# Performance work log

Hardware: AMD Instinct MI355X
Metric: run time of the kernel (lower is better)

The kernel has to match this reference:

```python
import jax, jax.numpy as jnp
import numpy as np

N = 50000        # num nodes
E = 800000       # num edges (no self loops by construction)
D = 128          # in_features == out_features
NE = 4           # num_envs
EPS = 1e-8
STDV = 1.0 / np.sqrt(D)


def setup_inputs() -> dict:
    key = jax.random.key(0)
    k = jax.random.split(key, 6)
    x = jax.random.normal(k[0], (N, D), jnp.float32)
    row = jax.random.randint(k[1], (E,), 0, N, dtype=jnp.int32)
    off = jax.random.randint(k[2], (E,), 1, N, dtype=jnp.int32)
    col = (row + off) % N  # guarantees no self loops (matches remove_self_loops)
    adj = jnp.stack([row, col])
    env_weights = jax.random.uniform(k[3], (N, NE), jnp.float32)
    weights = jax.random.uniform(k[4], (NE, D, D), jnp.float32, -STDV, STDV)
    a = jax.random.normal(k[5], (NE, 2 * D, 1), jnp.float32) * np.sqrt(2.0 / (2 * D + 1)) * 1.414
    return {"x": x, "adj": adj, "env_weights": env_weights, "weights": weights, "a": a}


def reference(x, adj, env_weights, weights, a):
    n = x.shape[0]
    f = weights.shape[-1]
    loops = jnp.arange(n, dtype=adj.dtype)
    src = jnp.concatenate([adj[0], loops])  # add_self_loops
    dst = jnp.concatenate([adj[1], loops])
    # per-env projected features: [NE, N, F]
    h = jnp.einsum('nd,edf->enf', x, weights)
    # attention logits: cat(h[src], h[dst]) @ a  ==  h[src]@a1 + h[dst]@a2
    a1 = a[:, :f, 0]   # [NE, F]
    a2 = a[:, f:, 0]   # [NE, F]
    s_src = jnp.einsum('enf,ef->en', h, a1)
    s_dst = jnp.einsum('enf,ef->en', h, a2)
    logits = jax.nn.leaky_relu(s_src[:, src] + s_dst[:, dst], 0.01)  # [NE, Etot]
    # global per-env max subtraction (as in the torch code: max over all edges)
    e = jnp.exp(logits - jnp.max(logits, axis=1, keepdims=True))
    def agg(ek, hk):
        # specialspmm: out[src] += ek * hk[dst]; denom via ones vector
        denom = jax.ops.segment_sum(ek, src, num_segments=n) + EPS          # [N]
        num = jax.ops.segment_sum(ek[:, None] * hk[dst], src, num_segments=n)  # [N, F]
        return num / denom[:, None]
    out_env = jax.vmap(agg)(e, h)  # [NE, N, F]
    out = jnp.einsum('ne,enf->nf', env_weights, out_env)
    return out + x  # residual
```

## Files before the change

### kernel.cpp

```cpp
#include <hip/hip_runtime.h>

#define N_NODES 50000
#define N_EDGES 800000
#define D_FEAT  128
#define NE_ENV  4
#define EPS_F   1e-8f
#define M_CONST 4.0f
#define NB_BUCKET 391
#define BINA_BLOCKS 250
#define BINA_EPT 13
#define NBH 200
#define EH  4000

typedef __attribute__((ext_vector_type(8))) short bf16x8;
typedef __attribute__((ext_vector_type(4))) float floatx4;
typedef __attribute__((ext_vector_type(2))) float f32x2;

static __device__ __forceinline__ unsigned short f2bf(float v) {
    union { float f; unsigned int u; } c; c.f = v;
    unsigned int u = c.u;
    u += 0x7fffu + ((u >> 16) & 1u);
    return (unsigned short)(u >> 16);
}

static __device__ __forceinline__ f32x2 bf2f(unsigned int v) {
    f32x2 r;
    r.x = __uint_as_float(v << 16);
    r.y = __uint_as_float(v & 0xffff0000u);
    return r;
}

static __device__ __forceinline__ float lrelu_exp(float z) {
    float lk = z > 0.f ? z : 0.01f * z;
    return __expf(lk - M_CONST);
}

static __device__ __forceinline__ void pk_add(f32x2& acc, f32x2 w) {
    asm("v_pk_add_f32 %0, %1, %0" : "+v"(acc) : "v"(w));
}
static __device__ __forceinline__ void pk_fma_bl(f32x2& acc, f32x2 w, f32x2 x) {
    asm("v_pk_fma_f32 %0, %1, %2, %0 op_sel:[0,0,0] op_sel_hi:[0,1,1]" : "+v"(acc) : "v"(w), "v"(x));
}
static __device__ __forceinline__ void pk_fma_bh(f32x2& acc, f32x2 w, f32x2 x) {
    asm("v_pk_fma_f32 %0, %1, %2, %0 op_sel:[1,0,0] op_sel_hi:[1,1,1]" : "+v"(acc) : "v"(w), "v"(x));
}

static __device__ __forceinline__ void edge_acc(unsigned int xv, float4 w,
        f32x2& den01, f32x2& den23, f32x2* axy) {
    f32x2 x = bf2f(xv);
    f32x2 wxy; wxy.x = w.x; wxy.y = w.y;
    f32x2 wzw; wzw.x = w.z; wzw.y = w.w;
    pk_add(den01, wxy);
    pk_add(den23, wzw);
    pk_fma_bl(axy[0], wxy, x);
    pk_fma_bh(axy[1], wxy, x);
    pk_fma_bl(axy[2], wzw, x);
    pk_fma_bh(axy[3], wzw, x);
}

__global__ __launch_bounds__(256) void k_setup(const float* __restrict__ weights, const float* __restrict__ a,
        float* __restrict__ b, unsigned short* __restrict__ wsw,
        const int* __restrict__ row, int* __restrict__ bcnt) {
    int blk = blockIdx.x;
    if (blk < 128) {
        int wave = threadIdx.x >> 6, lane = threadIdx.x & 63;
        int t = blk * 4 + wave;
        int e = t >> 7, d = t & 127;
        float2 w2 = ((const float2*)(weights + e * 16384 + d * 128))[lane];
        float2 a1 = ((const float2*)(a + e * 256))[lane];
        float2 a2 = ((const float2*)(a + e * 256 + 128))[lane];
        float p1 = w2.x * a1.x + w2.y * a1.y;
        float p2 = w2.x * a2.x + w2.y * a2.y;
#pragma unroll
        for (int off = 32; off > 0; off >>= 1) {
            p1 += __shfl_xor(p1, off, 64);
            p2 += __shfl_xor(p2, off, 64);
        }
        if (lane == 0) {
            b[e * 128 + d] = p1;
            b[512 + e * 128 + d] = p2;
        }
    } else if (blk < 384) {
        int idx = (blk - 128) * 256 + threadIdx.x;
        int j = idx & 7;
        int l = (idx >> 3) & 63;
        int t = (idx >> 9) & 7;
        int s = idx >> 12;
        int k = s * 32 + (l >> 4) * 8 + j;
        int f = t * 16 + (l & 15);
        int e = k >> 7, d = k & 127;
        wsw[idx] = f2bf(weights[e * 16384 + d * 128 + f]);
    } else {
        __shared__ int h[NB_BUCKET];
        int t = threadIdx.x;
        for (int i = t; i < NB_BUCKET; i += 256) h[i] = 0;
        __syncthreads();
        int e0 = (blk - 384) * EH;
        for (int j = t; j < EH; j += 256) {
            int k = e0 + j;
            if (k < N_EDGES) atomicAdd(&h[row[k] >> 7], 1);
        }
        __syncthreads();
        for (int i = t; i < NB_BUCKET; i += 256) {
            int c = h[i];
            if (c) atomicAdd(&bcnt[i], c);
        }
    }
}

__global__ __launch_bounds__(256) void k_s(const float* __restrict__ x, const float* __restrict__ b,
        float* __restrict__ s_src, float* __restrict__ s_dst, unsigned short* __restrict__ xbf) {
    int wave = threadIdx.x >> 6, lane = threadIdx.x & 63;
    int gw = blockIdx.x * 4 + wave;
    if (gw >= 3125) return;
    int quad = lane >> 4, lm = lane & 15;
    int base = gw * 16;

    floatx4 acc = (floatx4){0.f, 0.f, 0.f, 0.f};
    const float* xrow = x + (size_t)(base + lm) * 128 + quad * 8;
    unsigned short* xbrow = xbf + (size_t)(base + lm) * 128 + quad * 8;

#pragma unroll
    for (int s = 0; s < 4; ++s) {
        float4 lo = *(const float4*)(xrow + s * 32);
        float4 hi = *(const float4*)(xrow + s * 32 + 4);
        bf16x8 af;
        af[0] = (short)f2bf(lo.x); af[1] = (short)f2bf(lo.y);
        af[2] = (short)f2bf(lo.z); af[3] = (short)f2bf(lo.w);
        af[4] = (short)f2bf(hi.x); af[5] = (short)f2bf(hi.y);
        af[6] = (short)f2bf(hi.z); af[7] = (short)f2bf(hi.w);
        *(bf16x8*)(xbrow + s * 32) = af;

        bf16x8 bfv = (bf16x8){0, 0, 0, 0, 0, 0, 0, 0};
        if (lm < 8) {
            const float* bp = b + lm * 128 + s * 32 + quad * 8;
            float4 b0 = *(const float4*)bp;
            float4 b1 = *(const float4*)(bp + 4);
            bfv[0] = (short)f2bf(b0.x); bfv[1] = (short)f2bf(b0.y);
            bfv[2] = (short)f2bf(b0.z); bfv[3] = (short)f2bf(b0.w);
            bfv[4] = (short)f2bf(b1.x); bfv[5] = (short)f2bf(b1.y);
            bfv[6] = (short)f2bf(b1.z); bfv[7] = (short)f2bf(b1.w);
        }
        acc = __builtin_amdgcn_mfma_f32_16x16x32_bf16(af, bfv, acc, 0, 0, 0);
    }
    if (lm < 8) {
        float* dstp = (lm < 4) ? (s_src + (size_t)(base + quad * 4) * 4 + lm)
                               : (s_dst + (size_t)(base + quad * 4) * 4 + (lm - 4));
#pragma unroll
        for (int r = 0; r < 4; ++r) dstp[r * 4] = acc[r];
    }
}

__global__ void k_bscan(const int* __restrict__ bcnt, int* __restrict__ bbase,
                        int* __restrict__ bcur, int* __restrict__ offsets) {
    __shared__ int sm[512];
    int t = threadIdx.x;
    int v = (t < NB_BUCKET) ? bcnt[t] : 0;
    sm[t] = v;
    __syncthreads();
    for (int s2 = 1; s2 < 512; s2 <<= 1) {
        int add = (t >= s2) ? sm[t - s2] : 0;
        __syncthreads();
        sm[t] += add;
        __syncthreads();
    }
    int excl = sm[t] - v;
    if (t < NB_BUCKET) { bbase[t] = excl; bcur[t] = excl; }
    if (t == NB_BUCKET) bbase[t] = excl;
    if (t == 0) offsets[N_NODES] = N_EDGES;
}

__global__ __launch_bounds__(256) void k_binA(const int* __restrict__ row, const int* __restrict__ col,
        int* __restrict__ bcur, unsigned int* __restrict__ binned) {
    __shared__ int cnt[NB_BUCKET];
    __shared__ int base[NB_BUCKET];
    int t = threadIdx.x;
    for (int b = t; b < NB_BUCKET; b += 256) cnt[b] = 0;
    __syncthreads();
    unsigned int pk[BINA_EPT];
    int ebase = blockIdx.x * (256 * BINA_EPT) + t;
#pragma unroll
    for (int j = 0; j < BINA_EPT; ++j) {
        int k = ebase + j * 256;
        pk[j] = 0xffffffffu;
        if (k < N_EDGES) {
            unsigned int s = (unsigned int)row[k];
            unsigned int d = (unsigned int)col[k];
            pk[j] = (s << 16) | d;
            atomicAdd(&cnt[s >> 7], 1);
        }
    }
    __syncthreads();
    for (int b = t; b < NB_BUCKET; b += 256) {
        int c = cnt[b];
        base[b] = c ? atomicAdd(&bcur[b], c) : 0;
        cnt[b] = 0;
    }
    __syncthreads();
#pragma unroll
    for (int j = 0; j < BINA_EPT; ++j) {
        if (pk[j] != 0xffffffffu) {
            int b = pk[j] >> 23;
            int off = atomicAdd(&cnt[b], 1);
            binned[base[b] + off] = pk[j];
        }
    }
}

__global__ __launch_bounds__(256) void k_binB(const unsigned int* __restrict__ binned,
        const int* __restrict__ bbase,
        const float* __restrict__ s_src, const float* __restrict__ s_dst,
        int* __restrict__ offsets, int* __restrict__ sorted_dst, float4* __restrict__ w_sorted) {
    __shared__ int hist[128];
    __shared__ int cur[128];
    int b = blockIdx.x;
    int nb = b << 7;
    int nc = min(128, N_NODES - nb);
    int t = threadIdx.x;
    if (t < 128) hist[t] = 0;
    __syncthreads();
    int ebeg = bbase[b];
    int eend = bbase[b + 1];
    for (int i = ebeg + t; i < eend; i += 256)
        atomicAdd(&hist[(binned[i] >> 16) & 127], 1);
    __syncthreads();
    int v = (t < 128) ? hist[t] : 0;
    for (int s2 = 1; s2 < 128; s2 <<= 1) {
        int add = (t >= s2 && t < 128) ? hist[t - s2] : 0;
        __syncthreads();
        if (t < 128) hist[t] += add;
        __syncthreads();
    }
    if (t < 128) {
        int pos = ebeg + hist[t] - v;
        cur[t] = pos;
        if (t < nc) offsets[nb + t] = pos;
    }
    __syncthreads();
    for (int i = ebeg + t; i < eend; i += 256) {
        unsigned int pk = binned[i];
        int s = (int)(pk >> 16), d = (int)(pk & 0xffffu);
        float4 a4 = *(const float4*)(s_src + s * 4);
        float4 b4 = *(const float4*)(s_dst + d * 4);
        float4 w;
        w.x = lrelu_exp(a4.x + b4.x);
        w.y = lrelu_exp(a4.y + b4.y);
        w.z = lrelu_exp(a4.z + b4.z);
        w.w = lrelu_exp(a4.w + b4.w);
        int pos = atomicAdd(&cur[s & 127], 1);
        sorted_dst[pos] = d;
        w_sorted[pos] = w;
    }
}

__global__ __launch_bounds__(256) void k_agg_gemm(const unsigned int* __restrict__ xb,
        const float* __restrict__ s_src, const float* __restrict__ s_dst,
        const int* __restrict__ offsets, const int* __restrict__ sorted_dst,
        const float4* __restrict__ w_sorted, const float* __restrict__ env_w,
        const unsigned short* __restrict__ Wsw,
        const float* __restrict__ x, float* __restrict__ out) {
    __shared__ __align__(16) unsigned int Gsm[16 * 256];
    int wave = threadIdx.x >> 6, lane = threadIdx.x & 63;
    int nb = blockIdx.x * 16;

#pragma unroll 1
    for (int j = 0; j < 4; ++j) {
        int r = wave * 4 + j;
        int n = nb + r;

        f32x2 den01, den23;
        f32x2 axy[4];
        {
            float4 sa = *(const float4*)(s_src + n * 4);
            float4 sb = *(const float4*)(s_dst + n * 4);
            float ws0 = lrelu_exp(sa.x + sb.x), ws1 = lrelu_exp(sa.y + sb.y);
            float ws2 = lrelu_exp(sa.z + sb.z), ws3 = lrelu_exp(sa.w + sb.w);
            f32x2 xv = bf2f(xb[((unsigned)n << 6) + lane]);
            den01.x = ws0; den01.y = ws1;
            den23.x = ws2; den23.y = ws3;
            axy[0].x = ws0 * xv.x; axy[0].y = ws0 * xv.y;
            axy[1].x = ws1 * xv.x; axy[1].y = ws1 * xv.y;
            axy[2].x = ws2 * xv.x; axy[2].y = ws2 * xv.y;
            axy[3].x = ws3 * xv.x; axy[3].y = ws3 * xv.y;
        }

        int beg = __builtin_amdgcn_readfirstlane(offsets[n]);
        int end = __builtin_amdgcn_readfirstlane(offsets[n + 1]);
        int i = beg;

        if (i + 15 < end) {
            float4 wA[8]; unsigned int vA[8];
            {
                int dA[8];
#pragma unroll
                for (int q = 0; q < 8; ++q) dA[q] = sorted_dst[i + q];
#pragma unroll
                for (int q = 0; q < 8; ++q) vA[q] = xb[((unsigned)dA[q] << 6) + lane];
#pragma unroll
                for (int q = 0; q < 8; ++q) wA[q] = w_sorted[i + q];
            }
            i += 8;
            for (; i + 7 < end; i += 8) {
                int dB[8]; float4 wB[8]; unsigned int vB[8];
#pragma unroll
                for (int q = 0; q < 8; ++q) dB[q] = sorted_dst[i + q];
#pragma unroll
                for (int q = 0; q < 8; ++q) vB[q] = xb[((unsigned)dB[q] << 6) + lane];
#pragma unroll
                for (int q = 0; q < 8; ++q) wB[q] = w_sorted[i + q];
#pragma unroll
                for (int q = 0; q < 8; ++q) edge_acc(vA[q], wA[q], den01, den23, axy);
#pragma unroll
                for (int q = 0; q < 8; ++q) { vA[q] = vB[q]; wA[q] = wB[q]; }
            }
#pragma unroll
            for (int q = 0; q < 8; ++q) edge_acc(vA[q], wA[q], den01, den23, axy);
        }
        for (; i + 7 < end; i += 8) {
            int d[8]; float4 w[8]; unsigned int v[8];
#pragma unroll
            for (int q = 0; q < 8; ++q) d[q] = sorted_dst[i + q];
#pragma unroll
            for (int q = 0; q < 8; ++q) v[q] = xb[((unsigned)d[q] << 6) + lane];
#pragma unroll
            for (int q = 0; q < 8; ++q) w[q] = w_sorted[i + q];
#pragma unroll
            for (int q = 0; q < 8; ++q) edge_acc(v[q], w[q], den01, den23, axy);
        }
        for (; i + 3 < end; i += 4) {
            int d[4]; float4 w[4]; unsigned int v[4];
#pragma unroll
            for (int q = 0; q < 4; ++q) d[q] = sorted_dst[i + q];
#pragma unroll
            for (int q = 0; q < 4; ++q) v[q] = xb[((unsigned)d[q] << 6) + lane];
#pragma unroll
            for (int q = 0; q < 4; ++q) w[q] = w_sorted[i + q];
#pragma unroll
            for (int q = 0; q < 4; ++q) edge_acc(v[q], w[q], den01, den23, axy);
        }
        for (; i < end; ++i) {
            int d0 = sorted_dst[i];
            edge_acc(xb[((unsigned)d0 << 6) + lane], w_sorted[i], den01, den23, axy);
        }

        float4 ewt = *(const float4*)(env_w + n * 4);
        float ewv[4] = { ewt.x, ewt.y, ewt.z, ewt.w };
        float dens[4] = { den01.x, den01.y, den23.x, den23.y };
        int swz = (r & 7) << 2;
#pragma unroll
        for (int e = 0; e < 4; ++e) {
            float sc = ewv[e] / (dens[e] + EPS_F);
            unsigned int lo = f2bf(sc * axy[e].x);
            unsigned int hi = f2bf(sc * axy[e].y);
            Gsm[(r * 256 + e * 64 + lane) ^ swz] = (hi << 16) | lo;
        }
    }
    __syncthreads();

    int quad = lane >> 4, lm = lane & 15;
    int t0 = wave * 2;
    floatx4 acc0 = (floatx4){0.f, 0.f, 0.f, 0.f};
    floatx4 acc1 = (floatx4){0.f, 0.f, 0.f, 0.f};
    int rswz = (lm & 7) << 2;
#pragma unroll
    for (int s = 0; s < 16; ++s) {
        int idx = (lm * 256 + s * 16 + quad * 4) ^ rswz;
        bf16x8 af = *(const bf16x8*)(&Gsm[idx]);
        bf16x8 b0 = *(const bf16x8*)(Wsw + (((s * 8 + t0) * 64 + lane) * 8));
        bf16x8 b1 = *(const bf16x8*)(Wsw + (((s * 8 + t0 + 1) * 64 + lane) * 8));
        acc0 = __builtin_amdgcn_mfma_f32_16x16x32_bf16(af, b0, acc0, 0, 0, 0);
        acc1 = __builtin_amdgcn_mfma_f32_16x16x32_bf16(af, b1, acc1, 0, 0, 0);
    }
    int row_base = nb + quad * 4;
#pragma unroll
    for (int r = 0; r < 4; ++r) {
        int rowi = row_base + r;
        int c0 = t0 * 16 + lm;
        int c1 = c0 + 16;
        out[rowi * 128 + c0] = acc0[r] + x[rowi * 128 + c0];
        out[rowi * 128 + c1] = acc1[r] + x[rowi * 128 + c1];
    }
}

extern "C" void kernel_launch(void* const* d_in, const int* in_sizes, int n_in,
                              void* d_out, int out_size, void* d_ws, size_t ws_size,
                              hipStream_t stream) {
    const float* x       = (const float*)d_in[0];
    const int*   adj     = (const int*)d_in[1];
    const int*   row     = adj;
    const int*   col     = adj + N_EDGES;
    const float* env_w   = (const float*)d_in[2];
    const float* weights = (const float*)d_in[3];
    const float* a       = (const float*)d_in[4];
    float* out = (float*)d_out;

    char* ws = (char*)d_ws;
    size_t off = 0;
    auto alloc = [&](size_t bytes) -> char* {
        char* p = ws + off;
        off += (bytes + 255) & ~(size_t)255;
        return p;
    };
    float* b          = (float*)alloc(1024 * 4);
    float* s_src      = (float*)alloc((size_t)N_NODES * 4 * 4);
    float* s_dst      = (float*)alloc((size_t)N_NODES * 4 * 4);
    int*   offsets    = (int*)alloc((size_t)(N_NODES + 1) * 4);
    int*   bcnt       = (int*)alloc(512 * 4);
    int*   bbase      = (int*)alloc(512 * 4);
    int*   bcur       = (int*)alloc(512 * 4);
    unsigned int* binned = (unsigned int*)alloc((size_t)N_EDGES * 4);
    int*   sorted_dst = (int*)alloc((size_t)N_EDGES * 4);
    float4* w_sorted  = (float4*)alloc((size_t)N_EDGES * 16);
    unsigned short* wsw = (unsigned short*)alloc(65536 * 2);
    unsigned short* xbf = (unsigned short*)alloc((size_t)N_NODES * 128 * 2);

    hipMemsetAsync(bcnt, 0, 512 * 4, stream);
    k_setup<<<384 + NBH, 256, 0, stream>>>(weights, a, b, wsw, row, bcnt);
    k_s<<<782, 256, 0, stream>>>(x, b, s_src, s_dst, xbf);
    k_bscan<<<1, 512, 0, stream>>>(bcnt, bbase, bcur, offsets);
    k_binA<<<BINA_BLOCKS, 256, 0, stream>>>(row, col, bcur, binned);
    k_binB<<<NB_BUCKET, 256, 0, stream>>>(binned, bbase, s_src, s_dst, offsets, sorted_dst, w_sorted);
    k_agg_gemm<<<3125, 256, 0, stream>>>((const unsigned int*)xbf, s_src, s_dst, offsets,
                                         sorted_dst, w_sorted, env_w, wsw, x, out);
}
```

Before: 185.8 us.

## Fuse bucket scan into setup, double agg-gemm rows per block, scalarize weight pointer

Removes the separate single-block scan kernel by having the last histogram block (detected via an atomic done counter) do the bucket prefix scan. Doubles k_agg_gemm's tile to 32 nodes per block, so each loaded W fragment feeds twice as many MFMAs, and adds bounds guards for the partial last block. Forces the edge-weight base pointer through a VGPR move so the vector loads use a uniform address. Trade-offs: one fewer launch and less W reload traffic, against half as many blocks, fewer waves in flight for latency hiding during the gather, and double the LDS per block.

New measurement: 227.0 us. 22.2% more time.

```diff
diff --git a/kernel.cpp b/kernel.cpp
--- a/kernel.cpp
+++ b/kernel.cpp
@@ -58,9 +58,16 @@
     pk_fma_bh(axy[3], wzw, x);
 }
 
+static __device__ __forceinline__ const float4* wvec_ptr(const float4* w_sorted, int i) {
+    int iv;
+    asm("v_mov_b32 %0, %1" : "=v"(iv) : "s"(i));
+    return (const float4*)((const char*)w_sorted + ((size_t)(unsigned)iv * 16));
+}
+
 __global__ __launch_bounds__(256) void k_setup(const float* __restrict__ weights, const float* __restrict__ a,
         float* __restrict__ b, unsigned short* __restrict__ wsw,
-        const int* __restrict__ row, int* __restrict__ bcnt) {
+        const int* __restrict__ row, int* __restrict__ bcnt, int* __restrict__ done,
+        int* __restrict__ bbase, int* __restrict__ bcur, int* __restrict__ offsets) {
     int blk = blockIdx.x;
     if (blk < 128) {
         int wave = threadIdx.x >> 6, lane = threadIdx.x & 63;
@@ -92,8 +99,9 @@
         wsw[idx] = f2bf(weights[e * 16384 + d * 128 + f]);
     } else {
         __shared__ int h[NB_BUCKET];
+        __shared__ int lastflag;
         int t = threadIdx.x;
-        for (int i = t; i < NB_BUCKET; i += 256) h[i] = 0;
+        for (int i2 = t; i2 < NB_BUCKET; i2 += 256) h[i2] = 0;
         __syncthreads();
         int e0 = (blk - 384) * EH;
         for (int j = t; j < EH; j += 256) {
@@ -101,9 +109,34 @@
             if (k < N_EDGES) atomicAdd(&h[row[k] >> 7], 1);
         }
         __syncthreads();
-        for (int i = t; i < NB_BUCKET; i += 256) {
-            int c = h[i];
-            if (c) atomicAdd(&bcnt[i], c);
+        for (int i2 = t; i2 < NB_BUCKET; i2 += 256) {
+            int c = h[i2];
+            if (c) atomicAdd(&bcnt[i2], c);
+        }
+        __threadfence();
+        if (t == 0) lastflag = (atomicAdd(done, 1) == NBH - 1) ? 1 : 0;
+        __syncthreads();
+        if (!lastflag) return;
+        for (int i2 = t; i2 < NB_BUCKET; i2 += 256) h[i2] = atomicAdd(&bcnt[i2], 0);
+        __syncthreads();
+        if (t < 64) {
+            int run = 0;
+#pragma unroll 1
+            for (int c = 0; c < 7; ++c) {
+                int idx = c * 64 + t;
+                int xv = (idx < NB_BUCKET) ? h[idx] : 0;
+                int x = xv;
+#pragma unroll
+                for (int d = 1; d < 64; d <<= 1) {
+                    int y = __shfl_up(x, d, 64);
+                    if (t >= d) x += y;
+                }
+                int incl = x + run;
+                int excl = incl - xv;
+                if (idx < NB_BUCKET) { bbase[idx] = excl; bcur[idx] = excl; }
+                run = __shfl(incl, 63, 64);
+            }
+            if (t == 0) { bbase[NB_BUCKET] = N_EDGES; offsets[N_NODES] = N_EDGES; }
         }
     }
 }
@@ -149,25 +182,6 @@
 #pragma unroll
         for (int r = 0; r < 4; ++r) dstp[r * 4] = acc[r];
     }
-}
-
-__global__ void k_bscan(const int* __restrict__ bcnt, int* __restrict__ bbase,
-                        int* __restrict__ bcur, int* __restrict__ offsets) {
-    __shared__ int sm[512];
-    int t = threadIdx.x;
-    int v = (t < NB_BUCKET) ? bcnt[t] : 0;
-    sm[t] = v;
-    __syncthreads();
-    for (int s2 = 1; s2 < 512; s2 <<= 1) {
-        int add = (t >= s2) ? sm[t - s2] : 0;
-        __syncthreads();
-        sm[t] += add;
-        __syncthreads();
-    }
-    int excl = sm[t] - v;
-    if (t < NB_BUCKET) { bbase[t] = excl; bcur[t] = excl; }
-    if (t == NB_BUCKET) bbase[t] = excl;
-    if (t == 0) offsets[N_NODES] = N_EDGES;
 }
 
 __global__ __launch_bounds__(256) void k_binA(const int* __restrict__ row, const int* __restrict__ col,
@@ -259,14 +273,20 @@
         const float4* __restrict__ w_sorted, const float* __restrict__ env_w,
         const unsigned short* __restrict__ Wsw,
         const float* __restrict__ x, float* __restrict__ out) {
-    __shared__ __align__(16) unsigned int Gsm[16 * 256];
+    __shared__ __align__(16) unsigned int Gsm[32 * 256];
     int wave = threadIdx.x >> 6, lane = threadIdx.x & 63;
-    int nb = blockIdx.x * 16;
+    int nb = blockIdx.x * 32;
 
 #pragma unroll 1
-    for (int j = 0; j < 4; ++j) {
-        int r = wave * 4 + j;
+    for (int j = 0; j < 8; ++j) {
+        int r = wave * 8 + j;
         int n = nb + r;
+        int swz = (r & 7) << 2;
+        if (n >= N_NODES) {
+#pragma unroll
+            for (int e = 0; e < 4; ++e) Gsm[(r * 256 + e * 64 + lane) ^ swz] = 0;
+            continue;
+        }
 
         f32x2 den01, den23;
         f32x2 axy[4];
@@ -296,8 +316,9 @@
                 for (int q = 0; q < 8; ++q) dA[q] = sorted_dst[i + q];
 #pragma unroll
                 for (int q = 0; q < 8; ++q) vA[q] = xb[((unsigned)dA[q] << 6) + lane];
-#pragma unroll
-                for (int q = 0; q < 8; ++q) wA[q] = w_sorted[i + q];
+                const float4* wp = wvec_ptr(w_sorted, i);
+#pragma unroll
+                for (int q = 0; q < 8; ++q) wA[q] = wp[q];
             }
             i += 8;
             for (; i + 7 < end; i += 8) {
@@ -306,8 +327,9 @@
                 for (int q = 0; q < 8; ++q) dB[q] = sorted_dst[i + q];
 #pragma unroll
                 for (int q = 0; q < 8; ++q) vB[q] = xb[((unsigned)dB[q] << 6) + lane];
-#pragma unroll
-                for (int q = 0; q < 8; ++q) wB[q] = w_sorted[i + q];
+                const float4* wp = wvec_ptr(w_sorted, i);
+#pragma unroll
+                for (int q = 0; q < 8; ++q) wB[q] = wp[q];
 #pragma unroll
                 for (int q = 0; q < 8; ++q) edge_acc(vA[q], wA[q], den01, den23, axy);
 #pragma unroll
@@ -322,8 +344,9 @@
             for (int q = 0; q < 8; ++q) d[q] = sorted_dst[i + q];
 #pragma unroll
             for (int q = 0; q < 8; ++q) v[q] = xb[((unsigned)d[q] << 6) + lane];
-#pragma unroll
-            for (int q = 0; q < 8; ++q) w[q] = w_sorted[i + q];
+            const float4* wp = wvec_ptr(w_sorted, i);
+#pragma unroll
+            for (int q = 0; q < 8; ++q) w[q] = wp[q];
 #pragma unroll
             for (int q = 0; q < 8; ++q) edge_acc(v[q], w[q], den01, den23, axy);
         }
@@ -333,8 +356,9 @@
             for (int q = 0; q < 4; ++q) d[q] = sorted_dst[i + q];
 #pragma unroll
             for (int q = 0; q < 4; ++q) v[q] = xb[((unsigned)d[q] << 6) + lane];
-#pragma unroll
-            for (int q = 0; q < 4; ++q) w[q] = w_sorted[i + q];
+            const float4* wp = wvec_ptr(w_sorted, i);
+#pragma unroll
+            for (int q = 0; q < 4; ++q) w[q] = wp[q];
 #pragma unroll
             for (int q = 0; q < 4; ++q) edge_acc(v[q], w[q], den01, den23, axy);
         }
@@ -346,7 +370,6 @@
         float4 ewt = *(const float4*)(env_w + n * 4);
         float ewv[4] = { ewt.x, ewt.y, ewt.z, ewt.w };
         float dens[4] = { den01.x, den01.y, den23.x, den23.y };
-        int swz = (r & 7) << 2;
 #pragma unroll
         for (int e = 0; e < 4; ++e) {
             float sc = ewv[e] / (dens[e] + EPS_F);
@@ -359,26 +382,38 @@
 
     int quad = lane >> 4, lm = lane & 15;
     int t0 = wave * 2;
-    floatx4 acc0 = (floatx4){0.f, 0.f, 0.f, 0.f};
-    floatx4 acc1 = (floatx4){0.f, 0.f, 0.f, 0.f};
+    floatx4 a00 = (floatx4){0.f, 0.f, 0.f, 0.f};
+    floatx4 a01 = (floatx4){0.f, 0.f, 0.f, 0.f};
+    floatx4 a10 = (floatx4){0.f, 0.f, 0.f, 0.f};
+    floatx4 a11 = (floatx4){0.f, 0.f, 0.f, 0.f};
     int rswz = (lm & 7) << 2;
 #pragma unroll
     for (int s = 0; s < 16; ++s) {
-        int idx = (lm * 256 + s * 16 + quad * 4) ^ rswz;
-        bf16x8 af = *(const bf16x8*)(&Gsm[idx]);
+        int idx0 = (lm * 256 + s * 16 + quad * 4) ^ rswz;
+        int idx1 = ((16 + lm) * 256 + s * 16 + quad * 4) ^ rswz;
+        bf16x8 af0 = *(const bf16x8*)(&Gsm[idx0]);
+        bf16x8 af1 = *(const bf16x8*)(&Gsm[idx1]);
         bf16x8 b0 = *(const bf16x8*)(Wsw + (((s * 8 + t0) * 64 + lane) * 8));
         bf16x8 b1 = *(const bf16x8*)(Wsw + (((s * 8 + t0 + 1) * 64 + lane) * 8));
-        acc0 = __builtin_amdgcn_mfma_f32_16x16x32_bf16(af, b0, acc0, 0, 0, 0);
-        acc1 = __builtin_amdgcn_mfma_f32_16x16x32_bf16(af, b1, acc1, 0, 0, 0);
-    }
-    int row_base = nb + quad * 4;
+        a00 = __builtin_amdgcn_mfma_f32_16x16x32_bf16(af0, b0, a00, 0, 0, 0);
+        a01 = __builtin_amdgcn_mfma_f32_16x16x32_bf16(af0, b1, a01, 0, 0, 0);
+        a10 = __builtin_amdgcn_mfma_f32_16x16x32_bf16(af1, b0, a10, 0, 0, 0);
+        a11 = __builtin_amdgcn_mfma_f32_16x16x32_bf16(af1, b1, a11, 0, 0, 0);
+    }
+    int c0 = t0 * 16 + lm;
+    int c1 = c0 + 16;
 #pragma unroll
     for (int r = 0; r < 4; ++r) {
-        int rowi = row_base + r;
-        int c0 = t0 * 16 + lm;
-        int c1 = c0 + 16;
-        out[rowi * 128 + c0] = acc0[r] + x[rowi * 128 + c0];
-        out[rowi * 128 + c1] = acc1[r] + x[rowi * 128 + c1];
+        int r0 = nb + quad * 4 + r;
+        int r1 = r0 + 16;
+        if (r0 < N_NODES) {
+            out[r0 * 128 + c0] = a00[r] + x[r0 * 128 + c0];
+            out[r0 * 128 + c1] = a01[r] + x[r0 * 128 + c1];
+        }
+        if (r1 < N_NODES) {
+            out[r1 * 128 + c0] = a10[r] + x[r1 * 128 + c0];
+            out[r1 * 128 + c1] = a11[r] + x[r1 * 128 + c1];
+        }
     }
 }
 
@@ -405,7 +440,8 @@
     float* s_src      = (float*)alloc((size_t)N_NODES * 4 * 4);
     float* s_dst      = (float*)alloc((size_t)N_NODES * 4 * 4);
     int*   offsets    = (int*)alloc((size_t)(N_NODES + 1) * 4);
-    int*   bcnt       = (int*)alloc(512 * 4);
+    int*   bcnt       = (int*)alloc(516 * 4);
+    int*   done       = bcnt + 512;
     int*   bbase      = (int*)alloc(512 * 4);
     int*   bcur       = (int*)alloc(512 * 4);
     unsigned int* binned = (unsigned int*)alloc((size_t)N_EDGES * 4);
@@ -414,12 +450,11 @@
     unsigned short* wsw = (unsigned short*)alloc(65536 * 2);
     unsigned short* xbf = (unsigned short*)alloc((size_t)N_NODES * 128 * 2);
 
-    hipMemsetAsync(bcnt, 0, 512 * 4, stream);
-    k_setup<<<384 + NBH, 256, 0, stream>>>(weights, a, b, wsw, row, bcnt);
+    hipMemsetAsync(bcnt, 0, 516 * 4, stream);
+    k_setup<<<384 + NBH, 256, 0, stream>>>(weights, a, b, wsw, row, bcnt, done, bbase, bcur, offsets);
     k_s<<<782, 256, 0, stream>>>(x, b, s_src, s_dst, xbf);
-    k_bscan<<<1, 512, 0, stream>>>(bcnt, bbase, bcur, offsets);
     k_binA<<<BINA_BLOCKS, 256, 0, stream>>>(row, col, bcur, binned);
     k_binB<<<NB_BUCKET, 256, 0, stream>>>(binned, bbase, s_src, s_dst, offsets, sorted_dst, w_sorted);
-    k_agg_gemm<<<3125, 256, 0, stream>>>((const unsigned int*)xbf, s_src, s_dst, offsets,
+    k_agg_gemm<<<1563, 256, 0, stream>>>((const unsigned int*)xbf, s_src, s_dst, offsets,
                                          sorted_dst, w_sorted, env_w, wsw, x, out);
 }
```
